# Optimization experiments

Hardware: AMD Instinct MI355X
Metric: run time of the kernel (lower is better)

Reference implementation:

```python
import jax, jax.numpy as jnp
import numpy as np

DECAY = 0.99
EPS = 1e-05
COMMIT = 0.25


def setup_inputs() -> dict:
    key = jax.random.key(0)
    k1, k2 = jax.random.split(key)
    dim, n_embed = 256, 8192
    z = jax.random.normal(k1, (32, 32, 32, dim), dtype=jnp.float32)
    embed = jax.random.normal(k2, (dim, n_embed), dtype=jnp.float32)
    cluster_size = jnp.zeros((n_embed,), dtype=jnp.float32)
    embed_avg = embed  # torch init: embed_avg = embed.clone()
    return {"z": z, "embed": embed, "cluster_size": cluster_size, "embed_avg": embed_avg}


def reference(z, embed, cluster_size, embed_avg):
    dim, n_embed = embed.shape
    flatten = z.reshape(-1, dim)                       # [N, D]
    # squared L2 distance to each code: ||f||^2 - 2 f.E + ||E||^2
    dist = ((flatten ** 2).sum(1, keepdims=True)
            - 2.0 * flatten @ embed
            + (embed ** 2).sum(0, keepdims=True))      # [N, K]
    ind = jnp.argmin(dist, axis=1)                     # [N]
    quantize = jnp.take(embed.T, ind, axis=0).reshape(z.shape)
    embed_ind = ind.reshape(z.shape[:-1])

    # EMA codebook update (training mode), via segment_sum instead of a dense one-hot
    counts = jax.ops.segment_sum(jnp.ones_like(ind, dtype=flatten.dtype), ind,
                                 num_segments=n_embed)          # [K]
    embed_sum = jax.ops.segment_sum(flatten, ind,
                                    num_segments=n_embed).T     # [D, K]
    cluster_size_new = cluster_size * DECAY + (1.0 - DECAY) * counts
    embed_avg_new = embed_avg * DECAY + (1.0 - DECAY) * embed_sum
    n = cluster_size_new.sum()
    cs = (cluster_size_new + EPS) / (n + n_embed * EPS) * n
    embed_new = embed_avg_new / cs[None, :]

    diff = COMMIT * jnp.mean((jax.lax.stop_gradient(quantize) - z) ** 2)
    quantize_st = z + jax.lax.stop_gradient(quantize - z)  # straight-through
    return quantize_st, diff, embed_ind, embed_new
```

## Files before the change

### kernel.cpp

```cpp
#include <hip/hip_runtime.h>
#include <hip/hip_bf16.h>

#define D 256
#define K 8192
#define NTOT 32768
#define BM 128
#define BN2 128
#define BD 32
#define CSPLIT 4
#define CT_PER (K / CSPLIT / BN2)

typedef __bf16 bf16x8 __attribute__((ext_vector_type(8)));
typedef float f32x4 __attribute__((ext_vector_type(4)));

__device__ __forceinline__ void gl_lds16(const void* g, void* l) {
    __builtin_amdgcn_global_load_lds(
        (__attribute__((address_space(1))) void*)(g),
        (__attribute__((address_space(3))) void*)(l), 16, 0, 0);
}

__device__ __forceinline__ unsigned int enc_f32(float f) {
    unsigned int u = __float_as_uint(f);
    return (u & 0x80000000u) ? ~u : (u | 0x80000000u);
}

__device__ __forceinline__ unsigned short f2bfu(float x) {
    __hip_bfloat16 h = __float2bfloat16(x);
    return __builtin_bit_cast(unsigned short, h);
}
__device__ __forceinline__ float bfu2f(unsigned short u) {
    return __bfloat162float(__builtin_bit_cast(__hip_bfloat16, u));
}

__global__ __launch_bounds__(256)
void conv_F(const float* __restrict__ z, unsigned short* __restrict__ Fhi,
            unsigned short* __restrict__ Flo) {
    int i4 = blockIdx.x * 256 + threadIdx.x;
    float4 v = ((const float4*)z)[i4];
    ushort4 h, l;
    h.x = f2bfu(v.x); l.x = f2bfu(v.x - bfu2f(h.x));
    h.y = f2bfu(v.y); l.y = f2bfu(v.y - bfu2f(h.y));
    h.z = f2bfu(v.z); l.z = f2bfu(v.z - bfu2f(h.z));
    h.w = f2bfu(v.w); l.w = f2bfu(v.w - bfu2f(h.w));
    ((ushort4*)Fhi)[i4] = h;
    ((ushort4*)Flo)[i4] = l;
}

__global__ __launch_bounds__(256)
void conv_E(const float* __restrict__ E, unsigned short* __restrict__ EhiT,
            unsigned short* __restrict__ EloT, float* __restrict__ ET,
            float* __restrict__ enorm) {
    __shared__ float tile[64][65];
    int tid = threadIdx.x;
    int k0 = blockIdx.x * 64, d0 = blockIdx.y * 64;
#pragma unroll
    for (int it = 0; it < 16; ++it) {
        int idx = it * 256 + tid;
        int dr = idx >> 6, kc = idx & 63;
        tile[kc][dr] = E[(d0 + dr) * K + k0 + kc];
    }
    __syncthreads();
    float psum[4];
#pragma unroll
    for (int it = 0; it < 16; ++it) {
        int idx = it * 256 + tid;
        int kr = idx >> 6, dc = idx & 63;
        float v = tile[kr][dc];
        unsigned short h = f2bfu(v);
        int o = (k0 + kr) * D + d0 + dc;
        EhiT[o] = h;
        EloT[o] = f2bfu(v - bfu2f(h));
        ET[o] = v;
        psum[it & 3] = (it < 4 ? 0.f : psum[it & 3]) + v * v;
    }
#pragma unroll
    for (int g = 0; g < 4; ++g) {
        float p = psum[g];
#pragma unroll
        for (int off = 32; off; off >>= 1) p += __shfl_down(p, off);
        if ((tid & 63) == 0) {
            int kr = g * 4 + (tid >> 6);
            atomicAdd(&enorm[k0 + kr * 4 + 0], 0.f);
        }
    }
}

__global__ __launch_bounds__(256)
void enorm_kernel(const float* __restrict__ ET, float* __restrict__ enorm) {
    int k = blockIdx.x * 256 + threadIdx.x;
    const float4* row = (const float4*)(ET + k * D);
    float s = 0.f;
#pragma unroll
    for (int d = 0; d < D / 4; ++d) {
        float4 v = row[d];
        s += v.x * v.x + v.y * v.y + v.z * v.z + v.w * v.w;
    }
    enorm[k] = s;
}

__global__ __launch_bounds__(256)
void mfma_dist_argmin(const unsigned short* __restrict__ Fhi,
                      const unsigned short* __restrict__ Flo,
                      const unsigned short* __restrict__ EhiT,
                      const unsigned short* __restrict__ EloT,
                      const float* __restrict__ enorm,
                      unsigned long long* __restrict__ bestpack) {
    __shared__ unsigned short Ah[BM * BD], Al[BM * BD], Bh[BN2 * BD], Bl[BN2 * BD];

    const int tid = threadIdx.x;
    const int wave = tid >> 6;
    const int lane = tid & 63;
    const int qd = lane >> 4;
    const int ln = lane & 15;
    const int wm = (wave >> 1) * 64;
    const int wn = (wave & 1) * 64;
    const int n0 = blockIdx.x * BM;
    const int c0 = blockIdx.y * (K / CSPLIT);
    const int r_ = tid >> 2;
    const int s_sw = (tid & 3) ^ ((tid >> 3) & 3);
    const int csw = (qd ^ ((ln >> 1) & 3)) * 8;

    float bestv[16];
    int besti[16];
#pragma unroll
    for (int i = 0; i < 16; ++i) { bestv[i] = 3.402823466e38f; besti[i] = 0; }

    for (int ct = 0; ct < CT_PER; ++ct) {
        const int cb = c0 + ct * BN2;
        f32x4 acc[4][4];
#pragma unroll
        for (int mi = 0; mi < 4; ++mi)
#pragma unroll
            for (int ni = 0; ni < 4; ++ni) acc[mi][ni] = (f32x4){0.f, 0.f, 0.f, 0.f};

        for (int d0 = 0; d0 < D; d0 += BD) {
            __syncthreads();
#pragma unroll
            for (int it = 0; it < 2; ++it) {
                const int ga = (n0 + it * 64 + r_) * D + d0 + s_sw * 8;
                const int gb = (cb + it * 64 + r_) * D + d0 + s_sw * 8;
                const int lo = it * 2048 + wave * 512;
                gl_lds16(Fhi + ga, &Ah[lo]);
                gl_lds16(Flo + ga, &Al[lo]);
                gl_lds16(EhiT + gb, &Bh[lo]);
                gl_lds16(EloT + gb, &Bl[lo]);
            }
            __syncthreads();

            bf16x8 ah[4], al[4], bh[4], bl[4];
#pragma unroll
            for (int mi = 0; mi < 4; ++mi) {
                int off = (wm + mi * 16 + ln) * BD + csw;
                ah[mi] = *(const bf16x8*)&Ah[off];
                al[mi] = *(const bf16x8*)&Al[off];
            }
#pragma unroll
            for (int ni = 0; ni < 4; ++ni) {
                int off = (wn + ni * 16 + ln) * BD + csw;
                bh[ni] = *(const bf16x8*)&Bh[off];
                bl[ni] = *(const bf16x8*)&Bl[off];
            }
#pragma unroll
            for (int mi = 0; mi < 4; ++mi)
#pragma unroll
                for (int ni = 0; ni < 4; ++ni)
                    acc[mi][ni] = __builtin_amdgcn_mfma_f32_16x16x32_bf16(
                        ah[mi], bh[ni], acc[mi][ni], 0, 0, 0);
#pragma unroll
            for (int mi = 0; mi < 4; ++mi)
#pragma unroll
                for (int ni = 0; ni < 4; ++ni)
                    acc[mi][ni] = __builtin_amdgcn_mfma_f32_16x16x32_bf16(
                        ah[mi], bl[ni], acc[mi][ni], 0, 0, 0);
#pragma unroll
            for (int mi = 0; mi < 4; ++mi)
#pragma unroll
                for (int ni = 0; ni < 4; ++ni)
                    acc[mi][ni] = __builtin_amdgcn_mfma_f32_16x16x32_bf16(
                        al[mi], bh[ni], acc[mi][ni], 0, 0, 0);
        }

        float en[4];
#pragma unroll
        for (int ni = 0; ni < 4; ++ni) en[ni] = enorm[cb + wn + ni * 16 + ln];
#pragma unroll
        for (int ni = 0; ni < 4; ++ni) {
            int k = cb + wn + ni * 16 + ln;
#pragma unroll
            for (int mi = 0; mi < 4; ++mi) {
                f32x4 a = acc[mi][ni];
#pragma unroll
                for (int r = 0; r < 4; ++r) {
                    float dist = en[ni] - 2.0f * a[r];
                    int bi = mi * 4 + r;
                    if (dist < bestv[bi]) { bestv[bi] = dist; besti[bi] = k; }
                }
            }
        }
    }

#pragma unroll
    for (int mi = 0; mi < 4; ++mi) {
#pragma unroll
        for (int r = 0; r < 4; ++r) {
            int bi = mi * 4 + r;
            float v = bestv[bi];
            int ix = besti[bi];
#pragma unroll
            for (int off = 1; off < 16; off <<= 1) {
                float v2 = __shfl_xor(v, off);
                int i2 = __shfl_xor(ix, off);
                if (v2 < v || (v2 == v && i2 < ix)) { v = v2; ix = i2; }
            }
            if (ln == 0) {
                int m = n0 + wm + mi * 16 + qd * 4 + r;
                unsigned long long pack =
                    ((unsigned long long)enc_f32(v) << 32) | (unsigned int)ix;
                atomicMin(&bestpack[m], pack);
            }
        }
    }
}

#define ROWS_PER_BLOCK 64
__global__ __launch_bounds__(256)
void assign_apply(const float* __restrict__ z,
                  const float* __restrict__ ET,
                  const unsigned long long* __restrict__ bestpack,
                  float* __restrict__ out_q, float* __restrict__ out_ind,
                  float* __restrict__ out_diff,
                  float* __restrict__ counts, float* __restrict__ esumT) {
    const int tx = threadIdx.x;
    const int rbase = blockIdx.x * ROWS_PER_BLOCK;
    float part = 0.f;
    for (int r = 0; r < ROWS_PER_BLOCK; ++r) {
        int n = rbase + r;
        unsigned long long p = bestpack[n];
        int idx = (int)(p & 0xFFFFFFFFull);
        float f = z[n * D + tx];
        float q = ET[idx * D + tx];
        out_q[n * D + tx] = q;
        float dd = q - f;
        part += dd * dd;
        atomicAdd(&esumT[idx * D + tx], f);
        if (tx == 0) {
            atomicAdd(&counts[idx], 1.0f);
            out_ind[n] = (float)idx;
        }
    }
#pragma unroll
    for (int off = 32; off; off >>= 1) part += __shfl_down(part, off);
    __shared__ float wsum[4];
    if ((tx & 63) == 0) wsum[tx >> 6] = part;
    __syncthreads();
    if (tx == 0) {
        float t = wsum[0] + wsum[1] + wsum[2] + wsum[3];
        atomicAdd(out_diff, t * (0.25f / 8388608.0f));
    }
}

__global__ __launch_bounds__(1024)
void csn_sum(const float* __restrict__ cs_in, const float* __restrict__ counts,
             float* __restrict__ csn, float* __restrict__ nsum) {
    const float decay = 0.99f;
    const float omd = 0.01f;
    int tx = threadIdx.x;
    float p = 0.f;
    for (int k = tx; k < K; k += 1024) {
        float v = decay * cs_in[k] + omd * counts[k];
        csn[k] = v;
        p += v;
    }
#pragma unroll
    for (int off = 32; off; off >>= 1) p += __shfl_down(p, off);
    __shared__ float red[16];
    if ((tx & 63) == 0) red[tx >> 6] = p;
    __syncthreads();
    if (tx == 0) {
        float t = 0.f;
        for (int i = 0; i < 16; ++i) t += red[i];
        nsum[0] = t;
    }
}

__global__ __launch_bounds__(256)
void finalize(const float* __restrict__ eavg, const float* __restrict__ esumT,
              const float* __restrict__ csn, const float* __restrict__ nsum,
              float* __restrict__ out_enew) {
    const float decay = 0.99f;
    const float omd = 0.01f;
    const float keps = (float)(8192 * 1e-5);
    int idx = blockIdx.x * 256 + threadIdx.x;
    float nv = nsum[0];
    int k = idx & (K - 1);
    int d = idx >> 13;
    float avg_new = decay * eavg[idx] + omd * esumT[k * D + d];
    float cs = (csn[k] + 1e-5f) / (nv + keps) * nv;
    out_enew[idx] = avg_new / cs;
}

extern "C" void kernel_launch(void* const* d_in, const int* in_sizes, int n_in,
                              void* d_out, int out_size, void* d_ws, size_t ws_size,
                              hipStream_t stream) {
    const float* z = (const float*)d_in[0];
    const float* embed = (const float*)d_in[1];
    const float* cs_in = (const float*)d_in[2];
    const float* eavg = (const float*)d_in[3];

    float* out = (float*)d_out;
    float* out_q = out;
    float* out_diff = out + 8388608;
    float* out_ind = out + 8388609;
    float* out_enew = out + 8421377;

    char* ws = (char*)d_ws;
    unsigned long long* bestpack = (unsigned long long*)ws;
    float* enorm = (float*)(ws + 262144);
    float* counts = (float*)(ws + 294912);
    float* csn = (float*)(ws + 327680);
    float* nsum = (float*)(ws + 360448);
    float* esumT = (float*)(ws + 360704);
    unsigned short* Fhi = (unsigned short*)(ws + 8749312);
    unsigned short* Flo = (unsigned short*)(ws + 25526528);
    unsigned short* EhiT = (unsigned short*)(ws + 42303744);
    unsigned short* EloT = (unsigned short*)(ws + 46498048);
    float* ET = (float*)(ws + 50692352);

    hipMemsetAsync(bestpack, 0xFF, NTOT * 8, stream);
    hipMemsetAsync(counts, 0, K * 4, stream);
    hipMemsetAsync(esumT, 0, K * D * 4, stream);
    hipMemsetAsync(out_diff, 0, 4, stream);

    conv_F<<<NTOT * D / 4 / 256, 256, 0, stream>>>(z, Fhi, Flo);
    conv_E<<<dim3(K / 64, D / 64), 256, 0, stream>>>(embed, EhiT, EloT, ET, enorm);
    enorm_kernel<<<K / 256, 256, 0, stream>>>(ET, enorm);
    mfma_dist_argmin<<<dim3(NTOT / BM, CSPLIT), 256, 0, stream>>>(Fhi, Flo, EhiT, EloT,
                                                                  enorm, bestpack);
    assign_apply<<<NTOT / ROWS_PER_BLOCK, 256, 0, stream>>>(z, ET, bestpack, out_q,
                                                            out_ind, out_diff, counts, esumT);
    csn_sum<<<1, 1024, 0, stream>>>(cs_in, counts, csn, nsum);
    finalize<<<(D * K) / 256, 256, 0, stream>>>(eavg, esumT, csn, nsum, out_enew);
}
```

Baseline: 604.8 us.

## Double-buffer LDS tiles and switch distance GEMM to 32x32x16 MFMA

Restructures the distance/argmin GEMM into one flattened loop over codebook tiles and depth steps. The next tile is prefetched into a second LDS buffer while the current one is computed, with explicit vmcnt waits and raw barriers replacing the two syncthreads per step. The MFMA is switched from 16x16x32 to 32x32x16 with a new fragment layout and row mapping for the argmin reduction, and launch bounds request two blocks per CU. It also drops a dead atomicAdd loop from conv_E. The risks are doubled LDS use, more registers for 32-slot best tracking, and correctness of the new lane-to-row mapping.

```diff
diff --git a/kernel.cpp b/kernel.cpp
--- a/kernel.cpp
+++ b/kernel.cpp
@@ -9,9 +9,11 @@
 #define BD 32
 #define CSPLIT 4
 #define CT_PER (K / CSPLIT / BN2)
+#define NSTEP (CT_PER * (D / BD))
 
 typedef __bf16 bf16x8 __attribute__((ext_vector_type(8)));
 typedef float f32x4 __attribute__((ext_vector_type(4)));
+typedef float f32x16 __attribute__((ext_vector_type(16)));
 
 __device__ __forceinline__ void gl_lds16(const void* g, void* l) {
     __builtin_amdgcn_global_load_lds(
@@ -48,8 +50,7 @@
 
 __global__ __launch_bounds__(256)
 void conv_E(const float* __restrict__ E, unsigned short* __restrict__ EhiT,
-            unsigned short* __restrict__ EloT, float* __restrict__ ET,
-            float* __restrict__ enorm) {
+            unsigned short* __restrict__ EloT, float* __restrict__ ET) {
     __shared__ float tile[64][65];
     int tid = threadIdx.x;
     int k0 = blockIdx.x * 64, d0 = blockIdx.y * 64;
@@ -60,7 +61,6 @@
         tile[kc][dr] = E[(d0 + dr) * K + k0 + kc];
     }
     __syncthreads();
-    float psum[4];
 #pragma unroll
     for (int it = 0; it < 16; ++it) {
         int idx = it * 256 + tid;
@@ -71,17 +71,6 @@
         EhiT[o] = h;
         EloT[o] = f2bfu(v - bfu2f(h));
         ET[o] = v;
-        psum[it & 3] = (it < 4 ? 0.f : psum[it & 3]) + v * v;
-    }
-#pragma unroll
-    for (int g = 0; g < 4; ++g) {
-        float p = psum[g];
-#pragma unroll
-        for (int off = 32; off; off >>= 1) p += __shfl_down(p, off);
-        if ((tid & 63) == 0) {
-            int kr = g * 4 + (tid >> 6);
-            atomicAdd(&enorm[k0 + kr * 4 + 0], 0.f);
-        }
     }
 }
 
@@ -98,122 +87,161 @@
     enorm[k] = s;
 }
 
-__global__ __launch_bounds__(256)
+__global__ __launch_bounds__(256, 2)
 void mfma_dist_argmin(const unsigned short* __restrict__ Fhi,
                       const unsigned short* __restrict__ Flo,
                       const unsigned short* __restrict__ EhiT,
                       const unsigned short* __restrict__ EloT,
                       const float* __restrict__ enorm,
                       unsigned long long* __restrict__ bestpack) {
-    __shared__ unsigned short Ah[BM * BD], Al[BM * BD], Bh[BN2 * BD], Bl[BN2 * BD];
+    __shared__ __align__(16) unsigned short Ah[2][BM * BD];
+    __shared__ __align__(16) unsigned short Al[2][BM * BD];
+    __shared__ __align__(16) unsigned short Bh[2][BN2 * BD];
+    __shared__ __align__(16) unsigned short Bl[2][BN2 * BD];
 
     const int tid = threadIdx.x;
     const int wave = tid >> 6;
     const int lane = tid & 63;
-    const int qd = lane >> 4;
-    const int ln = lane & 15;
+    const int l5 = lane >> 5;
+    const int lr = lane & 31;
     const int wm = (wave >> 1) * 64;
     const int wn = (wave & 1) * 64;
     const int n0 = blockIdx.x * BM;
     const int c0 = blockIdx.y * (K / CSPLIT);
+
     const int r_ = tid >> 2;
     const int s_sw = (tid & 3) ^ ((tid >> 3) & 3);
-    const int csw = (qd ^ ((ln >> 1) & 3)) * 8;
-
-    float bestv[16];
-    int besti[16];
-#pragma unroll
-    for (int i = 0; i < 16; ++i) { bestv[i] = 3.402823466e38f; besti[i] = 0; }
-
-    for (int ct = 0; ct < CT_PER; ++ct) {
+
+    float bestv[32];
+    int besti[32];
+#pragma unroll
+    for (int i = 0; i < 32; ++i) { bestv[i] = 3.402823466e38f; besti[i] = 0; }
+
+    auto STAGE = [&](int b, int cb_, int d0_) {
+#pragma unroll
+        for (int it = 0; it < 2; ++it) {
+            const int ga = (n0 + it * 64 + r_) * D + d0_ + s_sw * 8;
+            const int gb = (cb_ + it * 64 + r_) * D + d0_ + s_sw * 8;
+            const int lo = it * 2048 + wave * 512;
+            gl_lds16(Fhi + ga, &Ah[b][lo]);
+            gl_lds16(Flo + ga, &Al[b][lo]);
+            gl_lds16(EhiT + gb, &Bh[b][lo]);
+            gl_lds16(EloT + gb, &Bl[b][lo]);
+        }
+    };
+
+    f32x16 acc[2][2];
+
+    STAGE(0, c0, 0);
+
+    for (int s = 0; s < NSTEP; ++s) {
+        const int cur = s & 1;
+        const int kk = s & 7;
+        const int ct = s >> 3;
         const int cb = c0 + ct * BN2;
-        f32x4 acc[4][4];
-#pragma unroll
-        for (int mi = 0; mi < 4; ++mi)
-#pragma unroll
-            for (int ni = 0; ni < 4; ++ni) acc[mi][ni] = (f32x4){0.f, 0.f, 0.f, 0.f};
-
-        for (int d0 = 0; d0 < D; d0 += BD) {
-            __syncthreads();
-#pragma unroll
-            for (int it = 0; it < 2; ++it) {
-                const int ga = (n0 + it * 64 + r_) * D + d0 + s_sw * 8;
-                const int gb = (cb + it * 64 + r_) * D + d0 + s_sw * 8;
-                const int lo = it * 2048 + wave * 512;
-                gl_lds16(Fhi + ga, &Ah[lo]);
-                gl_lds16(Flo + ga, &Al[lo]);
-                gl_lds16(EhiT + gb, &Bh[lo]);
-                gl_lds16(EloT + gb, &Bl[lo]);
-            }
-            __syncthreads();
-
-            bf16x8 ah[4], al[4], bh[4], bl[4];
-#pragma unroll
-            for (int mi = 0; mi < 4; ++mi) {
-                int off = (wm + mi * 16 + ln) * BD + csw;
-                ah[mi] = *(const bf16x8*)&Ah[off];
-                al[mi] = *(const bf16x8*)&Al[off];
-            }
-#pragma unroll
-            for (int ni = 0; ni < 4; ++ni) {
-                int off = (wn + ni * 16 + ln) * BD + csw;
-                bh[ni] = *(const bf16x8*)&Bh[off];
-                bl[ni] = *(const bf16x8*)&Bl[off];
-            }
-#pragma unroll
-            for (int mi = 0; mi < 4; ++mi)
-#pragma unroll
-                for (int ni = 0; ni < 4; ++ni)
-                    acc[mi][ni] = __builtin_amdgcn_mfma_f32_16x16x32_bf16(
-                        ah[mi], bh[ni], acc[mi][ni], 0, 0, 0);
-#pragma unroll
-            for (int mi = 0; mi < 4; ++mi)
-#pragma unroll
-                for (int ni = 0; ni < 4; ++ni)
-                    acc[mi][ni] = __builtin_amdgcn_mfma_f32_16x16x32_bf16(
-                        ah[mi], bl[ni], acc[mi][ni], 0, 0, 0);
-#pragma unroll
-            for (int mi = 0; mi < 4; ++mi)
-#pragma unroll
-                for (int ni = 0; ni < 4; ++ni)
-                    acc[mi][ni] = __builtin_amdgcn_mfma_f32_16x16x32_bf16(
-                        al[mi], bh[ni], acc[mi][ni], 0, 0, 0);
-        }
-
-        float en[4];
-#pragma unroll
-        for (int ni = 0; ni < 4; ++ni) en[ni] = enorm[cb + wn + ni * 16 + ln];
-#pragma unroll
-        for (int ni = 0; ni < 4; ++ni) {
-            int k = cb + wn + ni * 16 + ln;
-#pragma unroll
-            for (int mi = 0; mi < 4; ++mi) {
-                f32x4 a = acc[mi][ni];
-#pragma unroll
-                for (int r = 0; r < 4; ++r) {
-                    float dist = en[ni] - 2.0f * a[r];
-                    int bi = mi * 4 + r;
-                    if (dist < bestv[bi]) { bestv[bi] = dist; besti[bi] = k; }
+
+        if (s + 1 < NSTEP) {
+            const int s1 = s + 1;
+            STAGE(cur ^ 1, c0 + (s1 >> 3) * BN2, (s1 & 7) * BD);
+            asm volatile("s_waitcnt vmcnt(8)" ::: "memory");
+        } else {
+            asm volatile("s_waitcnt vmcnt(0)" ::: "memory");
+        }
+        __builtin_amdgcn_s_barrier();
+
+        if (kk == 0) {
+#pragma unroll
+            for (int mi = 0; mi < 2; ++mi)
+#pragma unroll
+                for (int ni = 0; ni < 2; ++ni)
+#pragma unroll
+                    for (int r = 0; r < 16; ++r) acc[mi][ni][r] = 0.f;
+        }
+
+        bf16x8 ah[2][2], al[2][2], bh[2][2], bl[2][2];
+#pragma unroll
+        for (int mi = 0; mi < 2; ++mi) {
+            const int row = wm + mi * 32 + lr;
+            const int rsw = (row >> 1) & 3;
+#pragma unroll
+            for (int ks = 0; ks < 2; ++ks) {
+                const int off = row * BD + ((ks * 2 + l5) ^ rsw) * 8;
+                ah[mi][ks] = *(const bf16x8*)&Ah[cur][off];
+                al[mi][ks] = *(const bf16x8*)&Al[cur][off];
+            }
+        }
+#pragma unroll
+        for (int ni = 0; ni < 2; ++ni) {
+            const int col = wn + ni * 32 + lr;
+            const int csw = (col >> 1) & 3;
+#pragma unroll
+            for (int ks = 0; ks < 2; ++ks) {
+                const int off = col * BD + ((ks * 2 + l5) ^ csw) * 8;
+                bh[ni][ks] = *(const bf16x8*)&Bh[cur][off];
+                bl[ni][ks] = *(const bf16x8*)&Bl[cur][off];
+            }
+        }
+
+#pragma unroll
+        for (int ks = 0; ks < 2; ++ks)
+#pragma unroll
+            for (int mi = 0; mi < 2; ++mi)
+#pragma unroll
+                for (int ni = 0; ni < 2; ++ni)
+                    acc[mi][ni] = __builtin_amdgcn_mfma_f32_32x32x16_bf16(
+                        ah[mi][ks], bh[ni][ks], acc[mi][ni], 0, 0, 0);
+#pragma unroll
+        for (int ks = 0; ks < 2; ++ks)
+#pragma unroll
+            for (int mi = 0; mi < 2; ++mi)
+#pragma unroll
+                for (int ni = 0; ni < 2; ++ni)
+                    acc[mi][ni] = __builtin_amdgcn_mfma_f32_32x32x16_bf16(
+                        ah[mi][ks], bl[ni][ks], acc[mi][ni], 0, 0, 0);
+#pragma unroll
+        for (int ks = 0; ks < 2; ++ks)
+#pragma unroll
+            for (int mi = 0; mi < 2; ++mi)
+#pragma unroll
+                for (int ni = 0; ni < 2; ++ni)
+                    acc[mi][ni] = __builtin_amdgcn_mfma_f32_32x32x16_bf16(
+                        al[mi][ks], bh[ni][ks], acc[mi][ni], 0, 0, 0);
+
+        if (kk == 7) {
+#pragma unroll
+            for (int ni = 0; ni < 2; ++ni) {
+                const int k = cb + wn + ni * 32 + lr;
+                const float en = enorm[k];
+#pragma unroll
+                for (int mi = 0; mi < 2; ++mi) {
+#pragma unroll
+                    for (int r = 0; r < 16; ++r) {
+                        const float dist = fmaf(-2.f, acc[mi][ni][r], en);
+                        const int slot = mi * 16 + r;
+                        if (dist < bestv[slot]) { bestv[slot] = dist; besti[slot] = k; }
+                    }
                 }
             }
         }
-    }
-
-#pragma unroll
-    for (int mi = 0; mi < 4; ++mi) {
-#pragma unroll
-        for (int r = 0; r < 4; ++r) {
-            int bi = mi * 4 + r;
-            float v = bestv[bi];
-            int ix = besti[bi];
-#pragma unroll
-            for (int off = 1; off < 16; off <<= 1) {
+        __builtin_amdgcn_s_barrier();
+    }
+
+#pragma unroll
+    for (int mi = 0; mi < 2; ++mi) {
+#pragma unroll
+        for (int r = 0; r < 16; ++r) {
+            const int slot = mi * 16 + r;
+            float v = bestv[slot];
+            int ix = besti[slot];
+#pragma unroll
+            for (int off = 1; off < 32; off <<= 1) {
                 float v2 = __shfl_xor(v, off);
                 int i2 = __shfl_xor(ix, off);
                 if (v2 < v || (v2 == v && i2 < ix)) { v = v2; ix = i2; }
             }
-            if (ln == 0) {
-                int m = n0 + wm + mi * 16 + qd * 4 + r;
+            if (lr == 0) {
+                const int row_local = (r & 3) + 8 * (r >> 2) + 4 * l5;
+                const int m = n0 + wm + mi * 32 + row_local;
                 unsigned long long pack =
                     ((unsigned long long)enc_f32(v) << 32) | (unsigned int)ix;
                 atomicMin(&bestpack[m], pack);
@@ -332,7 +360,7 @@
     hipMemsetAsync(out_diff, 0, 4, stream);
 
     conv_F<<<NTOT * D / 4 / 256, 256, 0, stream>>>(z, Fhi, Flo);
-    conv_E<<<dim3(K / 64, D / 64), 256, 0, stream>>>(embed, EhiT, EloT, ET, enorm);
+    conv_E<<<dim3(K / 64, D / 64), 256, 0, stream>>>(embed, EhiT, EloT, ET);
     enorm_kernel<<<K / 256, 256, 0, stream>>>(ET, enorm);
     mfma_dist_argmin<<<dim3(NTOT / BM, CSPLIT), 256, 0, stream>>>(Fhi, Flo, EhiT, EloT,
                                                                   enorm, bestpack);
```

New measurement: 669.5 us. 1.11x slower.

## Widen codebook tile to 256 with 8 waves and fold norm into accumulator init

Applied to the files above, without the earlier changes.

The distance/argmin kernel now runs 512 threads (8 waves in a 2x4 layout) over a 256-wide codebook tile, so each F tile loaded into LDS is reused across twice as many codes and there are half as many outer iterations. The accumulator starts at -0.5*||e||^2, so the argmin becomes an argmax on the raw accumulator and the per-element multiply-subtract in the epilogue goes away. The dead per-block enorm atomic loop in conv_E is also removed. The trade-offs are higher LDS use per block, changed occupancy under launch_bounds(512,4), and a slightly different rounding order for the norm term.

```diff
diff --git a/kernel.cpp b/kernel.cpp
--- a/kernel.cpp
+++ b/kernel.cpp
@@ -5,7 +5,7 @@
 #define K 8192
 #define NTOT 32768
 #define BM 128
-#define BN2 128
+#define BN2 256
 #define BD 32
 #define CSPLIT 4
 #define CT_PER (K / CSPLIT / BN2)
@@ -48,8 +48,7 @@
 
 __global__ __launch_bounds__(256)
 void conv_E(const float* __restrict__ E, unsigned short* __restrict__ EhiT,
-            unsigned short* __restrict__ EloT, float* __restrict__ ET,
-            float* __restrict__ enorm) {
+            unsigned short* __restrict__ EloT, float* __restrict__ ET) {
     __shared__ float tile[64][65];
     int tid = threadIdx.x;
     int k0 = blockIdx.x * 64, d0 = blockIdx.y * 64;
@@ -60,7 +59,6 @@
         tile[kc][dr] = E[(d0 + dr) * K + k0 + kc];
     }
     __syncthreads();
-    float psum[4];
 #pragma unroll
     for (int it = 0; it < 16; ++it) {
         int idx = it * 256 + tid;
@@ -71,17 +69,6 @@
         EhiT[o] = h;
         EloT[o] = f2bfu(v - bfu2f(h));
         ET[o] = v;
-        psum[it & 3] = (it < 4 ? 0.f : psum[it & 3]) + v * v;
-    }
-#pragma unroll
-    for (int g = 0; g < 4; ++g) {
-        float p = psum[g];
-#pragma unroll
-        for (int off = 32; off; off >>= 1) p += __shfl_down(p, off);
-        if ((tid & 63) == 0) {
-            int kr = g * 4 + (tid >> 6);
-            atomicAdd(&enorm[k0 + kr * 4 + 0], 0.f);
-        }
     }
 }
 
@@ -98,24 +85,26 @@
     enorm[k] = s;
 }
 
-__global__ __launch_bounds__(256)
+__global__ __launch_bounds__(512, 4)
 void mfma_dist_argmin(const unsigned short* __restrict__ Fhi,
                       const unsigned short* __restrict__ Flo,
                       const unsigned short* __restrict__ EhiT,
                       const unsigned short* __restrict__ EloT,
                       const float* __restrict__ enorm,
                       unsigned long long* __restrict__ bestpack) {
-    __shared__ unsigned short Ah[BM * BD], Al[BM * BD], Bh[BN2 * BD], Bl[BN2 * BD];
+    __shared__ __align__(16) unsigned short Ah[BM * BD], Al[BM * BD];
+    __shared__ __align__(16) unsigned short Bh[BN2 * BD], Bl[BN2 * BD];
 
     const int tid = threadIdx.x;
     const int wave = tid >> 6;
     const int lane = tid & 63;
     const int qd = lane >> 4;
     const int ln = lane & 15;
-    const int wm = (wave >> 1) * 64;
-    const int wn = (wave & 1) * 64;
+    const int wm = (wave >> 2) * 64;
+    const int wn = (wave & 3) * 64;
     const int n0 = blockIdx.x * BM;
     const int c0 = blockIdx.y * (K / CSPLIT);
+
     const int r_ = tid >> 2;
     const int s_sw = (tid & 3) ^ ((tid >> 3) & 3);
     const int csw = (qd ^ ((ln >> 1) & 3)) * 8;
@@ -123,25 +112,34 @@
     float bestv[16];
     int besti[16];
 #pragma unroll
-    for (int i = 0; i < 16; ++i) { bestv[i] = 3.402823466e38f; besti[i] = 0; }
+    for (int i = 0; i < 16; ++i) { bestv[i] = -3.402823466e38f; besti[i] = 0; }
 
     for (int ct = 0; ct < CT_PER; ++ct) {
         const int cb = c0 + ct * BN2;
+
+        float en[4];
+#pragma unroll
+        for (int ni = 0; ni < 4; ++ni) en[ni] = enorm[cb + wn + ni * 16 + ln];
+
         f32x4 acc[4][4];
 #pragma unroll
-        for (int mi = 0; mi < 4; ++mi)
-#pragma unroll
-            for (int ni = 0; ni < 4; ++ni) acc[mi][ni] = (f32x4){0.f, 0.f, 0.f, 0.f};
+        for (int ni = 0; ni < 4; ++ni) {
+            const float e = -0.5f * en[ni];
+#pragma unroll
+            for (int mi = 0; mi < 4; ++mi) acc[mi][ni] = (f32x4){e, e, e, e};
+        }
 
         for (int d0 = 0; d0 < D; d0 += BD) {
             __syncthreads();
+            {
+                const int ga = (n0 + r_) * D + d0 + s_sw * 8;
+                gl_lds16(Fhi + ga, &Ah[wave * 512]);
+                gl_lds16(Flo + ga, &Al[wave * 512]);
+            }
 #pragma unroll
             for (int it = 0; it < 2; ++it) {
-                const int ga = (n0 + it * 64 + r_) * D + d0 + s_sw * 8;
-                const int gb = (cb + it * 64 + r_) * D + d0 + s_sw * 8;
-                const int lo = it * 2048 + wave * 512;
-                gl_lds16(Fhi + ga, &Ah[lo]);
-                gl_lds16(Flo + ga, &Al[lo]);
+                const int gb = (cb + it * 128 + r_) * D + d0 + s_sw * 8;
+                const int lo = it * 4096 + wave * 512;
                 gl_lds16(EhiT + gb, &Bh[lo]);
                 gl_lds16(EloT + gb, &Bl[lo]);
             }
@@ -150,16 +148,17 @@
             bf16x8 ah[4], al[4], bh[4], bl[4];
 #pragma unroll
             for (int mi = 0; mi < 4; ++mi) {
-                int off = (wm + mi * 16 + ln) * BD + csw;
+                const int off = (wm + mi * 16 + ln) * BD + csw;
                 ah[mi] = *(const bf16x8*)&Ah[off];
                 al[mi] = *(const bf16x8*)&Al[off];
             }
 #pragma unroll
             for (int ni = 0; ni < 4; ++ni) {
-                int off = (wn + ni * 16 + ln) * BD + csw;
+                const int off = (wn + ni * 16 + ln) * BD + csw;
                 bh[ni] = *(const bf16x8*)&Bh[off];
                 bl[ni] = *(const bf16x8*)&Bl[off];
             }
+
 #pragma unroll
             for (int mi = 0; mi < 4; ++mi)
 #pragma unroll
@@ -180,20 +179,16 @@
                         al[mi], bh[ni], acc[mi][ni], 0, 0, 0);
         }
 
-        float en[4];
-#pragma unroll
-        for (int ni = 0; ni < 4; ++ni) en[ni] = enorm[cb + wn + ni * 16 + ln];
 #pragma unroll
         for (int ni = 0; ni < 4; ++ni) {
-            int k = cb + wn + ni * 16 + ln;
+            const int k = cb + wn + ni * 16 + ln;
 #pragma unroll
             for (int mi = 0; mi < 4; ++mi) {
-                f32x4 a = acc[mi][ni];
 #pragma unroll
                 for (int r = 0; r < 4; ++r) {
-                    float dist = en[ni] - 2.0f * a[r];
-                    int bi = mi * 4 + r;
-                    if (dist < bestv[bi]) { bestv[bi] = dist; besti[bi] = k; }
+                    const float a = acc[mi][ni][r];
+                    const int slot = mi * 4 + r;
+                    if (a > bestv[slot]) { bestv[slot] = a; besti[slot] = k; }
                 }
             }
         }
@@ -203,19 +198,20 @@
     for (int mi = 0; mi < 4; ++mi) {
 #pragma unroll
         for (int r = 0; r < 4; ++r) {
-            int bi = mi * 4 + r;
-            float v = bestv[bi];
-            int ix = besti[bi];
+            const int slot = mi * 4 + r;
+            float v = bestv[slot];
+            int ix = besti[slot];
 #pragma unroll
             for (int off = 1; off < 16; off <<= 1) {
                 float v2 = __shfl_xor(v, off);
                 int i2 = __shfl_xor(ix, off);
-                if (v2 < v || (v2 == v && i2 < ix)) { v = v2; ix = i2; }
+                if (v2 > v || (v2 == v && i2 < ix)) { v = v2; ix = i2; }
             }
             if (ln == 0) {
-                int m = n0 + wm + mi * 16 + qd * 4 + r;
+                const int m = n0 + wm + mi * 16 + qd * 4 + r;
+                const float dist = -2.0f * v;
                 unsigned long long pack =
-                    ((unsigned long long)enc_f32(v) << 32) | (unsigned int)ix;
+                    ((unsigned long long)enc_f32(dist) << 32) | (unsigned int)ix;
                 atomicMin(&bestpack[m], pack);
             }
         }
@@ -332,9 +328,9 @@
     hipMemsetAsync(out_diff, 0, 4, stream);
 
     conv_F<<<NTOT * D / 4 / 256, 256, 0, stream>>>(z, Fhi, Flo);
-    conv_E<<<dim3(K / 64, D / 64), 256, 0, stream>>>(embed, EhiT, EloT, ET, enorm);
+    conv_E<<<dim3(K / 64, D / 64), 256, 0, stream>>>(embed, EhiT, EloT, ET);
     enorm_kernel<<<K / 256, 256, 0, stream>>>(ET, enorm);
-    mfma_dist_argmin<<<dim3(NTOT / BM, CSPLIT), 256, 0, stream>>>(Fhi, Flo, EhiT, EloT,
+    mfma_dist_argmin<<<dim3(NTOT / BM, CSPLIT), 512, 0, stream>>>(Fhi, Flo, EhiT, EloT,
                                                                   enorm, bestpack);
     assign_apply<<<NTOT / ROWS_PER_BLOCK, 256, 0, stream>>>(z, ET, bestpack, out_q,
                                                             out_ind, out_diff, counts, esumT);
```

Result: slower. 826.0 us (+36.6%).

## Fuse prep kernels, compute enorm inline, vectorize assign, fold cluster-size sum into finalize

Applied to the files above, without the earlier changes.

Merges the z and codebook conversion kernels into one launch, computing codebook norms with wave reductions and atomics instead of a separate kernel. The sum of the old cluster sizes is taken during prep, using the fact that the counts total N, so the single-block csn_sum kernel is no longer needed. assign_apply switches to float4 loads with four rows in flight per block and writes per-block diff partials that finalize reduces. The memsets are merged into fewer calls. The aim is to cut launch count and serialization; in exchange the norms now depend on the order of float atomics.

```diff
diff --git a/kernel.cpp b/kernel.cpp
--- a/kernel.cpp
+++ b/kernel.cpp
@@ -33,26 +33,40 @@
 }
 
 __global__ __launch_bounds__(256)
-void conv_F(const float* __restrict__ z, unsigned short* __restrict__ Fhi,
-            unsigned short* __restrict__ Flo) {
-    int i4 = blockIdx.x * 256 + threadIdx.x;
-    float4 v = ((const float4*)z)[i4];
-    ushort4 h, l;
-    h.x = f2bfu(v.x); l.x = f2bfu(v.x - bfu2f(h.x));
-    h.y = f2bfu(v.y); l.y = f2bfu(v.y - bfu2f(h.y));
-    h.z = f2bfu(v.z); l.z = f2bfu(v.z - bfu2f(h.z));
-    h.w = f2bfu(v.w); l.w = f2bfu(v.w - bfu2f(h.w));
-    ((ushort4*)Fhi)[i4] = h;
-    ((ushort4*)Flo)[i4] = l;
-}
-
-__global__ __launch_bounds__(256)
-void conv_E(const float* __restrict__ E, unsigned short* __restrict__ EhiT,
-            unsigned short* __restrict__ EloT, float* __restrict__ ET,
-            float* __restrict__ enorm) {
+void prep(const float* __restrict__ z, const float* __restrict__ E,
+          const float* __restrict__ cs_in,
+          unsigned short* __restrict__ Fhi, unsigned short* __restrict__ Flo,
+          unsigned short* __restrict__ EhiT, unsigned short* __restrict__ EloT,
+          float* __restrict__ ET, float* __restrict__ enorm,
+          float* __restrict__ nsum) {
     __shared__ float tile[64][65];
-    int tid = threadIdx.x;
-    int k0 = blockIdx.x * 64, d0 = blockIdx.y * 64;
+    const int tid = threadIdx.x;
+    const int bid = blockIdx.x;
+
+    if (bid < 8192) {
+        int i4 = bid * 256 + tid;
+        float4 v = ((const float4*)z)[i4];
+        ushort4 h, l;
+        h.x = f2bfu(v.x); l.x = f2bfu(v.x - bfu2f(h.x));
+        h.y = f2bfu(v.y); l.y = f2bfu(v.y - bfu2f(h.y));
+        h.z = f2bfu(v.z); l.z = f2bfu(v.z - bfu2f(h.z));
+        h.w = f2bfu(v.w); l.w = f2bfu(v.w - bfu2f(h.w));
+        ((ushort4*)Fhi)[i4] = h;
+        ((ushort4*)Flo)[i4] = l;
+        return;
+    }
+
+    const int eb = bid - 8192;
+    const int k0 = (eb & 127) * 64;
+    const int d0 = (eb >> 7) * 64;
+
+    if (eb < 128 && tid < 64) {
+        float s = cs_in[k0 + tid];
+#pragma unroll
+        for (int off = 32; off; off >>= 1) s += __shfl_down(s, off);
+        if (tid == 0) atomicAdd(nsum, s);
+    }
+
 #pragma unroll
     for (int it = 0; it < 16; ++it) {
         int idx = it * 256 + tid;
@@ -60,7 +74,6 @@
         tile[kc][dr] = E[(d0 + dr) * K + k0 + kc];
     }
     __syncthreads();
-    float psum[4];
 #pragma unroll
     for (int it = 0; it < 16; ++it) {
         int idx = it * 256 + tid;
@@ -71,31 +84,11 @@
         EhiT[o] = h;
         EloT[o] = f2bfu(v - bfu2f(h));
         ET[o] = v;
-        psum[it & 3] = (it < 4 ? 0.f : psum[it & 3]) + v * v;
-    }
-#pragma unroll
-    for (int g = 0; g < 4; ++g) {
-        float p = psum[g];
-#pragma unroll
-        for (int off = 32; off; off >>= 1) p += __shfl_down(p, off);
-        if ((tid & 63) == 0) {
-            int kr = g * 4 + (tid >> 6);
-            atomicAdd(&enorm[k0 + kr * 4 + 0], 0.f);
-        }
-    }
-}
-
-__global__ __launch_bounds__(256)
-void enorm_kernel(const float* __restrict__ ET, float* __restrict__ enorm) {
-    int k = blockIdx.x * 256 + threadIdx.x;
-    const float4* row = (const float4*)(ET + k * D);
-    float s = 0.f;
-#pragma unroll
-    for (int d = 0; d < D / 4; ++d) {
-        float4 v = row[d];
-        s += v.x * v.x + v.y * v.y + v.z * v.z + v.w * v.w;
-    }
-    enorm[k] = s;
+        float ss = v * v;
+#pragma unroll
+        for (int off = 32; off; off >>= 1) ss += __shfl_down(ss, off);
+        if ((tid & 63) == 0) atomicAdd(&enorm[k0 + it * 4 + (tid >> 6)], ss);
+    }
 }
 
 __global__ __launch_bounds__(256)
@@ -228,22 +221,31 @@
                   const float* __restrict__ ET,
                   const unsigned long long* __restrict__ bestpack,
                   float* __restrict__ out_q, float* __restrict__ out_ind,
-                  float* __restrict__ out_diff,
-                  float* __restrict__ counts, float* __restrict__ esumT) {
+                  float* __restrict__ counts, float* __restrict__ esumT,
+                  float* __restrict__ diffpart) {
     const int tx = threadIdx.x;
+    const int l = tx & 63;
+    const int sub = tx >> 6;
     const int rbase = blockIdx.x * ROWS_PER_BLOCK;
+    const float4* z4 = (const float4*)z;
+    const float4* ET4 = (const float4*)ET;
+    float4* q4 = (float4*)out_q;
     float part = 0.f;
-    for (int r = 0; r < ROWS_PER_BLOCK; ++r) {
-        int n = rbase + r;
-        unsigned long long p = bestpack[n];
-        int idx = (int)(p & 0xFFFFFFFFull);
-        float f = z[n * D + tx];
-        float q = ET[idx * D + tx];
-        out_q[n * D + tx] = q;
-        float dd = q - f;
-        part += dd * dd;
-        atomicAdd(&esumT[idx * D + tx], f);
-        if (tx == 0) {
+    for (int r = sub; r < ROWS_PER_BLOCK; r += 4) {
+        const int n = rbase + r;
+        const unsigned long long p = bestpack[n];
+        const int idx = (int)(p & 0xFFFFFFFFull);
+        float4 f = z4[n * 64 + l];
+        float4 q = ET4[idx * 64 + l];
+        q4[n * 64 + l] = q;
+        float dx = q.x - f.x, dy = q.y - f.y, dz = q.z - f.z, dw = q.w - f.w;
+        part += dx * dx + dy * dy + dz * dz + dw * dw;
+        float* ep = esumT + idx * D + l * 4;
+        atomicAdd(ep + 0, f.x);
+        atomicAdd(ep + 1, f.y);
+        atomicAdd(ep + 2, f.z);
+        atomicAdd(ep + 3, f.w);
+        if (l == 0) {
             atomicAdd(&counts[idx], 1.0f);
             out_ind[n] = (float)idx;
         }
@@ -253,49 +255,32 @@
     __shared__ float wsum[4];
     if ((tx & 63) == 0) wsum[tx >> 6] = part;
     __syncthreads();
-    if (tx == 0) {
-        float t = wsum[0] + wsum[1] + wsum[2] + wsum[3];
-        atomicAdd(out_diff, t * (0.25f / 8388608.0f));
-    }
-}
-
-__global__ __launch_bounds__(1024)
-void csn_sum(const float* __restrict__ cs_in, const float* __restrict__ counts,
-             float* __restrict__ csn, float* __restrict__ nsum) {
-    const float decay = 0.99f;
-    const float omd = 0.01f;
-    int tx = threadIdx.x;
-    float p = 0.f;
-    for (int k = tx; k < K; k += 1024) {
-        float v = decay * cs_in[k] + omd * counts[k];
-        csn[k] = v;
-        p += v;
-    }
-#pragma unroll
-    for (int off = 32; off; off >>= 1) p += __shfl_down(p, off);
-    __shared__ float red[16];
-    if ((tx & 63) == 0) red[tx >> 6] = p;
-    __syncthreads();
-    if (tx == 0) {
-        float t = 0.f;
-        for (int i = 0; i < 16; ++i) t += red[i];
-        nsum[0] = t;
-    }
+    if (tx == 0) diffpart[blockIdx.x] = wsum[0] + wsum[1] + wsum[2] + wsum[3];
 }
 
 __global__ __launch_bounds__(256)
 void finalize(const float* __restrict__ eavg, const float* __restrict__ esumT,
-              const float* __restrict__ csn, const float* __restrict__ nsum,
-              float* __restrict__ out_enew) {
-    const float decay = 0.99f;
-    const float omd = 0.01f;
-    const float keps = (float)(8192 * 1e-5);
-    int idx = blockIdx.x * 256 + threadIdx.x;
-    float nv = nsum[0];
-    int k = idx & (K - 1);
-    int d = idx >> 13;
-    float avg_new = decay * eavg[idx] + omd * esumT[k * D + d];
-    float cs = (csn[k] + 1e-5f) / (nv + keps) * nv;
+              const float* __restrict__ cs_in, const float* __restrict__ counts,
+              const float* __restrict__ nsum, const float* __restrict__ diffpart,
+              float* __restrict__ out_enew, float* __restrict__ out_diff) {
+    const int tid = threadIdx.x;
+    if (blockIdx.x == 0) {
+        float p = diffpart[tid] + diffpart[tid + 256];
+#pragma unroll
+        for (int off = 32; off; off >>= 1) p += __shfl_down(p, off);
+        __shared__ float sred[4];
+        if ((tid & 63) == 0) sred[tid >> 6] = p;
+        __syncthreads();
+        if (tid == 0)
+            *out_diff = (sred[0] + sred[1] + sred[2] + sred[3]) * (0.25f / 8388608.0f);
+    }
+    const int idx = blockIdx.x * 256 + tid;
+    const float nv = 0.99f * nsum[0] + 0.01f * 32768.0f;
+    const int k = idx & (K - 1);
+    const int d = idx >> 13;
+    const float csn_k = 0.99f * cs_in[k] + 0.01f * counts[k];
+    const float avg_new = 0.99f * eavg[idx] + 0.01f * esumT[k * D + d];
+    const float cs = (csn_k + 1e-5f) / (nv + 0.08192f) * nv;
     out_enew[idx] = avg_new / cs;
 }
 
@@ -317,27 +302,25 @@
     unsigned long long* bestpack = (unsigned long long*)ws;
     float* enorm = (float*)(ws + 262144);
     float* counts = (float*)(ws + 294912);
-    float* csn = (float*)(ws + 327680);
-    float* nsum = (float*)(ws + 360448);
-    float* esumT = (float*)(ws + 360704);
-    unsigned short* Fhi = (unsigned short*)(ws + 8749312);
-    unsigned short* Flo = (unsigned short*)(ws + 25526528);
-    unsigned short* EhiT = (unsigned short*)(ws + 42303744);
-    unsigned short* EloT = (unsigned short*)(ws + 46498048);
-    float* ET = (float*)(ws + 50692352);
-
-    hipMemsetAsync(bestpack, 0xFF, NTOT * 8, stream);
-    hipMemsetAsync(counts, 0, K * 4, stream);
-    hipMemsetAsync(esumT, 0, K * D * 4, stream);
-    hipMemsetAsync(out_diff, 0, 4, stream);
-
-    conv_F<<<NTOT * D / 4 / 256, 256, 0, stream>>>(z, Fhi, Flo);
-    conv_E<<<dim3(K / 64, D / 64), 256, 0, stream>>>(embed, EhiT, EloT, ET, enorm);
-    enorm_kernel<<<K / 256, 256, 0, stream>>>(ET, enorm);
+    float* nsum = (float*)(ws + 327680);
+    float* diffpart = (float*)(ws + 329728);
+    float* esumT = (float*)(ws + 331776);
+    unsigned short* Fhi = (unsigned short*)(ws + 8720384);
+    unsigned short* Flo = (unsigned short*)(ws + 25497600);
+    unsigned short* EhiT = (unsigned short*)(ws + 42274816);
+    unsigned short* EloT = (unsigned short*)(ws + 46469120);
+    float* ET = (float*)(ws + 50663424);
+
+    hipMemsetAsync(bestpack, 0xFF, 262144, stream);
+    hipMemsetAsync(ws + 262144, 0, 331776 - 262144 + 8388608, stream);
+
+    prep<<<8192 + 512, 256, 0, stream>>>(z, embed, cs_in, Fhi, Flo, EhiT, EloT, ET,
+                                         enorm, nsum);
     mfma_dist_argmin<<<dim3(NTOT / BM, CSPLIT), 256, 0, stream>>>(Fhi, Flo, EhiT, EloT,
                                                                   enorm, bestpack);
     assign_apply<<<NTOT / ROWS_PER_BLOCK, 256, 0, stream>>>(z, ET, bestpack, out_q,
-                                                            out_ind, out_diff, counts, esumT);
-    csn_sum<<<1, 1024, 0, stream>>>(cs_in, counts, csn, nsum);
-    finalize<<<(D * K) / 256, 256, 0, stream>>>(eavg, esumT, csn, nsum, out_enew);
-}
+                                                            out_ind, counts, esumT,
+                                                            diffpart);
+    finalize<<<(D * K) / 256, 256, 0, stream>>>(eavg, esumT, cs_in, counts, nsum,
+                                                diffpart, out_enew, out_diff);
+}
```

After: 707.0 us. 1.17x slower.
